# Kernel optimization log

Hardware: AMD Instinct MI355X
Metric: run time of the kernel (lower is better)

The kernel has to match this reference:

```python
import jax, jax.numpy as jnp
import numpy as np

B, C, D, H, K = 512, 112, 128, 8, 8  # batch, channels(=seq), d_model, heads, conv kernel
HD = D // H
SCALE = HD ** -0.5
BN_EPS = 1e-5
LN_EPS = 1e-5


def setup_inputs() -> dict:
    key = jax.random.key(0)
    ks = jax.random.split(key, 12)
    s = 0.05
    return {
        "x": jax.random.normal(ks[0], (B, C, D), jnp.float32),
        "conv_w": jax.random.normal(ks[1], (C, 1, K), jnp.float32) * s,
        "conv_b": jax.random.normal(ks[2], (C,), jnp.float32) * s,
        "bn_g": jnp.ones((C,), jnp.float32),
        "bn_b": jnp.zeros((C,), jnp.float32),
        "bn_m": jnp.zeros((C,), jnp.float32),
        "bn_v": jnp.ones((C,), jnp.float32),
        "wq": jax.random.normal(ks[3], (D, D), jnp.float32) * s,
        "bq": jax.random.normal(ks[4], (D,), jnp.float32) * s,
        "wk": jax.random.normal(ks[5], (D, D), jnp.float32) * s,
        "bk": jax.random.normal(ks[6], (D,), jnp.float32) * s,
        "wv": jax.random.normal(ks[7], (D, D), jnp.float32) * s,
        "bv": jax.random.normal(ks[8], (D,), jnp.float32) * s,
        "wo": jax.random.normal(ks[9], (D, D), jnp.float32) * s,
        "bo": jax.random.normal(ks[10], (D,), jnp.float32) * s,
        "ln_g": jnp.ones((D,), jnp.float32),
        "ln_b": jnp.zeros((D,), jnp.float32),
    }


def _forward(x, conv_w, conv_b, bn_g, bn_b, bn_m, bn_v,
             wq, bq, wk, bk, wv, bv, wo, bo, ln_g, ln_b):
    # resnet_1: depthwise Conv1d(padding='same', k=8) -> GELU -> BatchNorm1d (eval)
    # torch 'same' padding for even k: left = (k-1)//2 = 3, right = 4
    h = jax.lax.conv_general_dilated(
        x, conv_w, window_strides=(1,), padding=[(3, 4)],
        dimension_numbers=("NCH", "OIH", "NCH"), feature_group_count=C)
    h = h + conv_b[None, :, None]
    h = jax.nn.gelu(h, approximate=False)
    h = (h - bn_m[None, :, None]) * (bn_g[None, :, None] * jax.lax.rsqrt(bn_v + BN_EPS)[None, :, None]) + bn_b[None, :, None]
    src = x + h  # [B, C, D]; attention treats C as sequence dim

    # multi-head attention (hand-rolled, res_attention path with prev=None)
    q = (src @ wq.T + bq).reshape(B, C, H, HD).transpose(0, 2, 1, 3)  # [B,H,S,hd]
    k = (src @ wk.T + bk).reshape(B, C, H, HD).transpose(0, 2, 1, 3)
    v = (src @ wv.T + bv).reshape(B, C, H, HD).transpose(0, 2, 1, 3)
    scores = jnp.einsum("bhqd,bhkd->bhqk", q, k) * SCALE  # [B,H,S,S]
    attn = jax.nn.softmax(scores, axis=-1)
    out = jnp.einsum("bhqk,bhkd->bhqd", attn, v)  # [B,H,S,hd]
    out = out.transpose(0, 2, 1, 3).reshape(B, C, D)
    out = out @ wo.T + bo

    # residual + LayerNorm over last dim
    src = src + out
    mu = jnp.mean(src, axis=-1, keepdims=True)
    var = jnp.mean(jnp.square(src - mu), axis=-1, keepdims=True)
    src = (src - mu) * jax.lax.rsqrt(var + LN_EPS) * ln_g + ln_b
    return src


def reference(x, conv_w, conv_b, bn_g, bn_b, bn_m, bn_v,
              wq, bq, wk, bk, wv, bv, wo, bo, ln_g, ln_b):
    return _forward(x, conv_w, conv_b, bn_g, bn_b, bn_m, bn_v,
                    wq, bq, wk, bk, wv, bv, wo, bo, ln_g, ln_b)
```

## Files before the change

### kernel.cpp

```cpp
#include <hip/hip_runtime.h>
#include <hip/hip_bf16.h>

#define BB 512
#define CC 112
#define DD 128
#define HH 8
#define HD 16
#define KK 8
#define SROW 140

typedef unsigned short u16;
typedef short short8 __attribute__((ext_vector_type(8)));
typedef float f32x4 __attribute__((ext_vector_type(4)));
typedef float f32x16 __attribute__((ext_vector_type(16)));

#define MFMA16(a, b, c) __builtin_amdgcn_mfma_f32_16x16x32_bf16(a, b, c, 0, 0, 0)
#define MFMA32(a, b, c) __builtin_amdgcn_mfma_f32_32x32x16_bf16(a, b, c, 0, 0, 0)

#define GLD_LDS16(gsrc, ldst)                                          \
  __builtin_amdgcn_global_load_lds(                                    \
      (const __attribute__((address_space(1))) char*)(gsrc),           \
      (__attribute__((address_space(3))) char*)(ldst), 16, 0, 0)

__device__ inline u16 f2bf(float f) {
  union { float f; unsigned u; } v{f};
  unsigned r = (v.u + 0x7FFFu + ((v.u >> 16) & 1u)) >> 16;
  return (u16)r;
}
__device__ inline float bf2f(u16 u) {
  union { unsigned u; float f; } v;
  v.u = ((unsigned)u) << 16;
  return v.f;
}
__device__ inline unsigned pk2(float a, float b) {
  __hip_bfloat162 h = __float22bfloat162_rn(float2{a, b});
  union { __hip_bfloat162 h; unsigned u; } v{h};
  return v.u;
}

__device__ inline unsigned permx32(unsigned x) {
  unsigned a = x, b = x;
  asm("v_permlane32_swap_b32 %0, %1" : "+v"(a), "+v"(b));
  return (threadIdx.x & 32) ? a : b;
}
__device__ inline float permx32f(float x) {
  union { float f; unsigned u; } v{x};
  v.u = permx32(v.u);
  return v.f;
}

__global__ __launch_bounds__(256) void k_wcvt(
    const float* __restrict__ wq, const float* __restrict__ wk,
    const float* __restrict__ wv, const float* __restrict__ wo,
    u16* __restrict__ w_b) {
  const int i = (blockIdx.x * 256 + threadIdx.x);
  const int sel = i >> 12, off = i & 4095;
  const float* w = (sel == 0) ? wq : (sel == 1) ? wk : (sel == 2) ? wv : wo;
  const float4 v = ((const float4*)w)[off];
  ((uint2*)w_b)[i] = uint2{pk2(v.x, v.y), pk2(v.z, v.w)};
}

__global__ __launch_bounds__(512, 4) void k_cqkv(
    const float* __restrict__ x, const float* __restrict__ cw,
    const float* __restrict__ cb, const float* __restrict__ bg,
    const float* __restrict__ bb_, const float* __restrict__ bm,
    const float* __restrict__ bv, const u16* __restrict__ w_b,
    const float* __restrict__ bq, const float* __restrict__ bk,
    const float* __restrict__ bvv,
    u16* __restrict__ src_b, u16* __restrict__ qb, u16* __restrict__ kb,
    u16* __restrict__ vtb) {
  __shared__ u16 S[CC * SROW];
  const int b = blockIdx.x;
  const int t = threadIdx.x;

  const int tg = t >> 2, sub = t & 3;
  if (tg < CC) {
    const int row = tg, ch = tg;
    const float4 w0 = *(const float4*)(cw + ch * KK);
    const float4 w1 = *(const float4*)(cw + ch * KK + 4);
    const float cbv = cb[ch];
    const float bscale = bg[ch] * rsqrtf(bv[ch] + 1e-5f);
    const float bmv = bm[ch], bbv = bb_[ch];
    const float* __restrict__ xr = x + ((size_t)b * CC + row) * DD;
    float in[40];
#pragma unroll
    for (int f = 0; f < 10; ++f) {
      const int fi = 8 * sub - 1 + f;
      float4 vv = {0.f, 0.f, 0.f, 0.f};
      if (fi >= 0 && fi < 32) vv = ((const float4*)xr)[fi];
      in[f * 4 + 0] = vv.x; in[f * 4 + 1] = vv.y;
      in[f * 4 + 2] = vv.z; in[f * 4 + 3] = vv.w;
    }
    unsigned pkv[16];
#pragma unroll
    for (int i2 = 0; i2 < 16; ++i2) {
      float oo[2];
#pragma unroll
      for (int j = 0; j < 2; ++j) {
        const int i = i2 * 2 + j;
        float a = 0.f;
        a = fmaf(in[i + 1], w0.x, a);
        a = fmaf(in[i + 2], w0.y, a);
        a = fmaf(in[i + 3], w0.z, a);
        a = fmaf(in[i + 4], w0.w, a);
        a = fmaf(in[i + 5], w1.x, a);
        a = fmaf(in[i + 6], w1.y, a);
        a = fmaf(in[i + 7], w1.z, a);
        a = fmaf(in[i + 8], w1.w, a);
        a += cbv;
        const float u = fmaf(0.044715f * a, a, 1.0f);
        const float e = __expf(a * u * -1.5957691216f);
        const float g = a * __frcp_rn(1.f + e);
        oo[j] = in[i + 4] + (g - bmv) * bscale + bbv;
      }
      pkv[i2] = pk2(oo[0], oo[1]);
    }
    u16* srow = S + row * SROW + sub * 32;
#pragma unroll
    for (int k2 = 0; k2 < 8; ++k2)
      *(uint2*)(srow + k2 * 4) = ((uint2*)pkv)[k2];
    uint4* gsr = (uint4*)(src_b + ((size_t)b * CC + row) * DD + sub * 32);
#pragma unroll
    for (int k4 = 0; k4 < 4; ++k4) gsr[k4] = ((uint4*)pkv)[k4];
  }
  __syncthreads();

  const int wave = t >> 6, lane = t & 63;
  const int quad = lane >> 4, n = lane & 15;
  const int h = wave;
  short8 Bf0[4], Bf1[4], Bf2[4];
#pragma unroll
  for (int kf = 0; kf < 4; ++kf) {
    const int wi = (h * 16 + n) * DD + kf * 32 + quad * 8;
    Bf0[kf] = *(const short8*)(w_b + wi);
    Bf1[kf] = *(const short8*)(w_b + 16384 + wi);
    Bf2[kf] = *(const short8*)(w_b + 32768 + wi);
  }
  const float bqv = bq[h * 16 + n];
  const float bkv = bk[h * 16 + n];
  const float bvv2 = bvv[h * 16 + n];
  u16* __restrict__ qhp = qb + (size_t)(b * HH + h) * CC * HD;
  u16* __restrict__ khp = kb + (size_t)(b * HH + h) * CC * HD;
  u16* __restrict__ vhp = vtb + (size_t)(b * HH + h) * HD * CC;
#pragma unroll
  for (int mt = 0; mt < 7; ++mt) {
    short8 A[4];
#pragma unroll
    for (int kf = 0; kf < 4; ++kf)
      A[kf] = *(const short8*)&S[(mt * 16 + n) * SROW + kf * 32 + quad * 8];
    f32x4 aq = {0.f, 0.f, 0.f, 0.f};
    f32x4 ak = {0.f, 0.f, 0.f, 0.f};
    f32x4 av = {0.f, 0.f, 0.f, 0.f};
#pragma unroll
    for (int kf = 0; kf < 4; ++kf) {
      aq = MFMA16(A[kf], Bf0[kf], aq);
      ak = MFMA16(A[kf], Bf1[kf], ak);
      av = MFMA16(A[kf], Bf2[kf], av);
    }
#pragma unroll
    for (int r = 0; r < 4; ++r) {
      const int row = mt * 16 + quad * 4 + r;
      qhp[row * HD + n] = f2bf(aq[r] + bqv);
      khp[row * HD + n] = f2bf(ak[r] + bkv);
      vhp[n * CC + row] = f2bf(av[r] + bvv2);
    }
  }
}

__global__ __launch_bounds__(512, 4) void k_attno(
    const u16* __restrict__ qb_, const u16* __restrict__ kb_,
    const u16* __restrict__ vtb_, const u16* __restrict__ w_bo,
    const float* __restrict__ bo, const u16* __restrict__ src_b,
    const float* __restrict__ lg, const float* __restrict__ lb,
    float* __restrict__ out) {
  __shared__ __attribute__((aligned(16))) u16 KL[HH * CC * HD];
  __shared__ __attribute__((aligned(16))) u16 VL[HH * HD * CC];
  __shared__ u16 AO[64 * SROW];
  const int bid = blockIdx.x;
  const int b = bid & (BB - 1);
  const int hb = bid >> 9;
  const int t = threadIdx.x;
  const int wave = t >> 6, lane = t & 63;

  {
    const char* kg = (const char*)(kb_ + (size_t)b * (HH * CC * HD));
    const char* vg = (const char*)(vtb_ + (size_t)b * (HH * HD * CC));
    char* kl = (char*)KL;
    char* vl = (char*)VL;
#pragma unroll
    for (int c0 = 0; c0 < 4; ++c0) {
      const int c = wave + c0 * 8;
      if (c < 28) {
        GLD_LDS16(kg + c * 1024 + (lane << 4), kl + c * 1024);
        GLD_LDS16(vg + c * 1024 + (lane << 4), vl + c * 1024);
      }
    }
  }
  __syncthreads();

  {
    const int h = wave;
    const int lo = lane & 31, hi = lane >> 5, hi8 = hi * 8;
    const u16* __restrict__ qh = qb_ + (size_t)(b * HH + h) * CC * HD;
    const u16* kh = KL + h * CC * HD;
    const u16* vth = VL + h * HD * CC;
    for (int qi = 0; qi < 2; ++qi) {
      const int qt = 2 * hb + qi;
      const int qt0 = qt * 32;
      short8 Bq = {};
      if (qt0 + lo < CC) Bq = *(const short8*)(qh + (qt0 + lo) * HD + hi8);
      f32x16 sa[4];
#pragma unroll
      for (int mt = 0; mt < 4; ++mt) {
        short8 Ak = {};
        const int key = mt * 32 + lo;
        if (key < CC) Ak = *(const short8*)(kh + key * HD + hi8);
        f32x16 z = {};
        sa[mt] = MFMA32(Ak, Bq, z);
      }
      const float C1 = 0.25f * 1.44269504088896341f;
      float mxp[4] = {-1e30f, -1e30f, -1e30f, -1e30f};
#pragma unroll
      for (int mt = 0; mt < 4; ++mt) {
        const int rmax = (mt == 3) ? 8 : 16;
#pragma unroll
        for (int r = 0; r < 16; ++r)
          if (r < rmax) mxp[r & 3] = fmaxf(mxp[r & 3], sa[mt][r]);
      }
      float mx = fmaxf(fmaxf(mxp[0], mxp[1]), fmaxf(mxp[2], mxp[3]));
      mx = fmaxf(mx, permx32f(mx));
      const float mxc = mx * C1;
      float sp[4] = {0.f, 0.f, 0.f, 0.f};
#pragma unroll
      for (int mt = 0; mt < 4; ++mt) {
        const int rmax = (mt == 3) ? 8 : 16;
#pragma unroll
        for (int r = 0; r < 16; ++r)
          if (r < rmax) {
            const float p = exp2f(fmaf(sa[mt][r], C1, -mxc));
            sa[mt][r] = p;
            sp[r & 3] += p;
          }
      }
      float sum = (sp[0] + sp[1]) + (sp[2] + sp[3]);
      sum += permx32f(sum);
      const float rinv = 1.f / sum;
      unsigned U0[4][4], U1[4][4];
#pragma unroll
      for (int mt = 0; mt < 4; ++mt) {
        const int rqmax = (mt == 3) ? 2 : 4;
#pragma unroll
        for (int rq = 0; rq < 4; ++rq)
          if (rq < rqmax) {
            U0[mt][rq] =
                pk2(sa[mt][4 * rq + 0] * rinv, sa[mt][4 * rq + 1] * rinv);
            U1[mt][rq] =
                pk2(sa[mt][4 * rq + 2] * rinv, sa[mt][4 * rq + 3] * rinv);
          }
      }
      f32x16 oacc = {};
#pragma unroll
      for (int kt = 0; kt < 7; ++kt) {
        const int mt = kt >> 1;
        const int c = 2 * (kt & 1);
        const unsigned own0 = hi ? U0[mt][c + 1] : U0[mt][c];
        const unsigned own1 = hi ? U1[mt][c + 1] : U1[mt][c];
        const unsigned snd0 = hi ? U0[mt][c] : U0[mt][c + 1];
        const unsigned snd1 = hi ? U1[mt][c] : U1[mt][c + 1];
        const unsigned got0 = permx32(snd0);
        const unsigned got1 = permx32(snd1);
        union { unsigned u[4]; short8 s; } ap;
        ap.u[0] = hi ? got0 : own0;
        ap.u[1] = hi ? got1 : own1;
        ap.u[2] = hi ? own0 : got0;
        ap.u[3] = hi ? own1 : got1;
        short8 Bv = {};
        if (lo < HD) Bv = *(const short8*)(vth + lo * CC + kt * 16 + hi8);
        oacc = MFMA32(ap.s, Bv, oacc);
      }
      if (lo < HD) {
#pragma unroll
        for (int r = 0; r < 16; ++r) {
          const int rr = (r & 3) + 8 * (r >> 2) + 4 * hi;
          if (qt0 + rr < CC)
            AO[(qi * 32 + rr) * SROW + h * HD + lo] = f2bf(oacc[r]);
        }
      }
    }
  }
  __syncthreads();

  if (wave < 4) {
    const int mt = 4 * hb + wave;
    if (mt < 7) {
      const int quad = lane >> 4, n = lane & 15;
      short8 A[4];
#pragma unroll
      for (int kf = 0; kf < 4; ++kf)
        A[kf] =
            *(const short8*)&AO[(wave * 16 + n) * SROW + kf * 32 + quad * 8];
      float v[8][4];
#pragma unroll
      for (int nt = 0; nt < 8; ++nt) {
        f32x4 acc = {0.f, 0.f, 0.f, 0.f};
#pragma unroll
        for (int kf = 0; kf < 4; ++kf) {
          const short8 Bf =
              *(const short8*)(w_bo + (nt * 16 + n) * DD + kf * 32 + quad * 8);
          acc = MFMA16(A[kf], Bf, acc);
        }
        const int col = nt * 16 + n;
        const float bcol = bo[col];
#pragma unroll
        for (int r = 0; r < 4; ++r)
          v[nt][r] =
              acc[r] + bcol +
              bf2f(src_b[((size_t)b * CC + mt * 16 + quad * 4 + r) * DD + col]);
      }
      float sum[4] = {0.f, 0.f, 0.f, 0.f}, sq[4] = {0.f, 0.f, 0.f, 0.f};
#pragma unroll
      for (int nt = 0; nt < 8; ++nt)
#pragma unroll
        for (int r = 0; r < 4; ++r) {
          sum[r] += v[nt][r];
          sq[r] = fmaf(v[nt][r], v[nt][r], sq[r]);
        }
#pragma unroll
      for (int d = 1; d < 16; d <<= 1)
#pragma unroll
        for (int r = 0; r < 4; ++r) {
          sum[r] += __shfl_xor(sum[r], d);
          sq[r] += __shfl_xor(sq[r], d);
        }
      float mu[4], rs[4];
#pragma unroll
      for (int r = 0; r < 4; ++r) {
        mu[r] = sum[r] * (1.f / DD);
        const float var = sq[r] * (1.f / DD) - mu[r] * mu[r];
        rs[r] = rsqrtf(var + 1e-5f);
      }
#pragma unroll
      for (int nt = 0; nt < 8; ++nt) {
        const int col = nt * 16 + n;
        const float g = lg[col], be = lb[col];
#pragma unroll
        for (int r = 0; r < 4; ++r)
          out[((size_t)b * CC + mt * 16 + quad * 4 + r) * DD + col] =
              (v[nt][r] - mu[r]) * rs[r] * g + be;
      }
    }
  }
}

extern "C" void kernel_launch(void* const* d_in, const int* in_sizes, int n_in,
                              void* d_out, int out_size, void* d_ws,
                              size_t ws_size, hipStream_t stream) {
  (void)in_sizes; (void)n_in; (void)out_size; (void)ws_size;
  const float* x   = (const float*)d_in[0];
  const float* cw  = (const float*)d_in[1];
  const float* cb  = (const float*)d_in[2];
  const float* bg  = (const float*)d_in[3];
  const float* bb  = (const float*)d_in[4];
  const float* bm  = (const float*)d_in[5];
  const float* bv  = (const float*)d_in[6];
  const float* wq  = (const float*)d_in[7];
  const float* bq  = (const float*)d_in[8];
  const float* wk  = (const float*)d_in[9];
  const float* bk  = (const float*)d_in[10];
  const float* wv  = (const float*)d_in[11];
  const float* bvv = (const float*)d_in[12];
  const float* wo  = (const float*)d_in[13];
  const float* bo  = (const float*)d_in[14];
  const float* lg  = (const float*)d_in[15];
  const float* lb  = (const float*)d_in[16];
  float* out = (float*)d_out;

  const size_t NE = (size_t)BB * CC * DD;
  u16* ub = (u16*)d_ws;
  u16* src_b = ub;
  u16* q_b   = ub + NE;
  u16* k_b   = ub + 2 * NE;
  u16* vt_b  = ub + 3 * NE;
  u16* w_b   = ub + 4 * NE;

  k_wcvt<<<64, 256, 0, stream>>>(wq, wk, wv, wo, w_b);
  k_cqkv<<<BB, 512, 0, stream>>>(x, cw, cb, bg, bb, bm, bv, w_b, bq, bk, bvv,
                                 src_b, q_b, k_b, vt_b);
  k_attno<<<2 * BB, 512, 0, stream>>>(q_b, k_b, vt_b, w_b + 3 * 16384, bo,
                                      src_b, lg, lb, out);
}
```

Baseline: 172.3 us.

## Fuse conv/QKV and attention/out-proj kernels into one per-batch kernel

```diff
diff --git a/kernel.cpp b/kernel.cpp
--- a/kernel.cpp
+++ b/kernel.cpp
@@ -8,6 +8,7 @@
 #define HD 16
 #define KK 8
 #define SROW 140
+#define QS 1792
 
 typedef unsigned short u16;
 typedef short short8 __attribute__((ext_vector_type(8)));
@@ -16,11 +17,6 @@
 
 #define MFMA16(a, b, c) __builtin_amdgcn_mfma_f32_16x16x32_bf16(a, b, c, 0, 0, 0)
 #define MFMA32(a, b, c) __builtin_amdgcn_mfma_f32_32x32x16_bf16(a, b, c, 0, 0, 0)
-
-#define GLD_LDS16(gsrc, ldst)                                          \
-  __builtin_amdgcn_global_load_lds(                                    \
-      (const __attribute__((address_space(1))) char*)(gsrc),           \
-      (__attribute__((address_space(3))) char*)(ldst), 16, 0, 0)
 
 __device__ inline u16 f2bf(float f) {
   union { float f; unsigned u; } v{f};
@@ -60,20 +56,24 @@
   ((uint2*)w_b)[i] = uint2{pk2(v.x, v.y), pk2(v.z, v.w)};
 }
 
-__global__ __launch_bounds__(512, 4) void k_cqkv(
+__global__ __launch_bounds__(1024, 4) void k_fused(
     const float* __restrict__ x, const float* __restrict__ cw,
     const float* __restrict__ cb, const float* __restrict__ bg,
     const float* __restrict__ bb_, const float* __restrict__ bm,
     const float* __restrict__ bv, const u16* __restrict__ w_b,
     const float* __restrict__ bq, const float* __restrict__ bk,
-    const float* __restrict__ bvv,
-    u16* __restrict__ src_b, u16* __restrict__ qb, u16* __restrict__ kb,
-    u16* __restrict__ vtb) {
-  __shared__ u16 S[CC * SROW];
+    const float* __restrict__ bvv, const float* __restrict__ bo,
+    const float* __restrict__ lg, const float* __restrict__ lb,
+    float* __restrict__ out) {
+  __shared__ __attribute__((aligned(16))) u16 S[CC * SROW];
+  __shared__ __attribute__((aligned(16))) u16 QL[HH * CC * HD];
+  __shared__ __attribute__((aligned(16))) u16 KL[HH * CC * HD];
+  __shared__ __attribute__((aligned(16))) u16 VTL[HH * HD * CC];
   const int b = blockIdx.x;
   const int t = threadIdx.x;
-
-  const int tg = t >> 2, sub = t & 3;
+  const int wave = t >> 6, lane = t & 63;
+
+  const int tg = t >> 3, s = t & 7;
   if (tg < CC) {
     const int row = tg, ch = tg;
     const float4 w0 = *(const float4*)(cw + ch * KK);
@@ -82,18 +82,18 @@
     const float bscale = bg[ch] * rsqrtf(bv[ch] + 1e-5f);
     const float bmv = bm[ch], bbv = bb_[ch];
     const float* __restrict__ xr = x + ((size_t)b * CC + row) * DD;
-    float in[40];
-#pragma unroll
-    for (int f = 0; f < 10; ++f) {
-      const int fi = 8 * sub - 1 + f;
+    float in[24];
+#pragma unroll
+    for (int f = 0; f < 6; ++f) {
+      const int fi = 4 * s - 1 + f;
       float4 vv = {0.f, 0.f, 0.f, 0.f};
       if (fi >= 0 && fi < 32) vv = ((const float4*)xr)[fi];
       in[f * 4 + 0] = vv.x; in[f * 4 + 1] = vv.y;
       in[f * 4 + 2] = vv.z; in[f * 4 + 3] = vv.w;
     }
-    unsigned pkv[16];
-#pragma unroll
-    for (int i2 = 0; i2 < 16; ++i2) {
+    unsigned pkv[8];
+#pragma unroll
+    for (int i2 = 0; i2 < 8; ++i2) {
       float oo[2];
 #pragma unroll
       for (int j = 0; j < 2; ++j) {
@@ -115,106 +115,79 @@
       }
       pkv[i2] = pk2(oo[0], oo[1]);
     }
-    u16* srow = S + row * SROW + sub * 32;
-#pragma unroll
-    for (int k2 = 0; k2 < 8; ++k2)
+    u16* srow = S + row * SROW + s * 16;
+#pragma unroll
+    for (int k2 = 0; k2 < 4; ++k2)
       *(uint2*)(srow + k2 * 4) = ((uint2*)pkv)[k2];
-    uint4* gsr = (uint4*)(src_b + ((size_t)b * CC + row) * DD + sub * 32);
-#pragma unroll
-    for (int k4 = 0; k4 < 4; ++k4) gsr[k4] = ((uint4*)pkv)[k4];
   }
   __syncthreads();
 
-  const int wave = t >> 6, lane = t & 63;
-  const int quad = lane >> 4, n = lane & 15;
-  const int h = wave;
-  short8 Bf0[4], Bf1[4], Bf2[4];
-#pragma unroll
-  for (int kf = 0; kf < 4; ++kf) {
-    const int wi = (h * 16 + n) * DD + kf * 32 + quad * 8;
-    Bf0[kf] = *(const short8*)(w_b + wi);
-    Bf1[kf] = *(const short8*)(w_b + 16384 + wi);
-    Bf2[kf] = *(const short8*)(w_b + 32768 + wi);
-  }
-  const float bqv = bq[h * 16 + n];
-  const float bkv = bk[h * 16 + n];
-  const float bvv2 = bvv[h * 16 + n];
-  u16* __restrict__ qhp = qb + (size_t)(b * HH + h) * CC * HD;
-  u16* __restrict__ khp = kb + (size_t)(b * HH + h) * CC * HD;
-  u16* __restrict__ vhp = vtb + (size_t)(b * HH + h) * HD * CC;
-#pragma unroll
-  for (int mt = 0; mt < 7; ++mt) {
-    short8 A[4];
-#pragma unroll
-    for (int kf = 0; kf < 4; ++kf)
-      A[kf] = *(const short8*)&S[(mt * 16 + n) * SROW + kf * 32 + quad * 8];
-    f32x4 aq = {0.f, 0.f, 0.f, 0.f};
-    f32x4 ak = {0.f, 0.f, 0.f, 0.f};
-    f32x4 av = {0.f, 0.f, 0.f, 0.f};
+  {
+    const int h = wave >> 1, mh = wave & 1;
+    const int quad = lane >> 4, n = lane & 15;
+    short8 Bf0[4], Bf1[4], Bf2[4];
 #pragma unroll
     for (int kf = 0; kf < 4; ++kf) {
-      aq = MFMA16(A[kf], Bf0[kf], aq);
-      ak = MFMA16(A[kf], Bf1[kf], ak);
-      av = MFMA16(A[kf], Bf2[kf], av);
-    }
-#pragma unroll
-    for (int r = 0; r < 4; ++r) {
-      const int row = mt * 16 + quad * 4 + r;
-      qhp[row * HD + n] = f2bf(aq[r] + bqv);
-      khp[row * HD + n] = f2bf(ak[r] + bkv);
-      vhp[n * CC + row] = f2bf(av[r] + bvv2);
-    }
-  }
-}
-
-__global__ __launch_bounds__(512, 4) void k_attno(
-    const u16* __restrict__ qb_, const u16* __restrict__ kb_,
-    const u16* __restrict__ vtb_, const u16* __restrict__ w_bo,
-    const float* __restrict__ bo, const u16* __restrict__ src_b,
-    const float* __restrict__ lg, const float* __restrict__ lb,
-    float* __restrict__ out) {
-  __shared__ __attribute__((aligned(16))) u16 KL[HH * CC * HD];
-  __shared__ __attribute__((aligned(16))) u16 VL[HH * HD * CC];
-  __shared__ u16 AO[64 * SROW];
-  const int bid = blockIdx.x;
-  const int b = bid & (BB - 1);
-  const int hb = bid >> 9;
-  const int t = threadIdx.x;
-  const int wave = t >> 6, lane = t & 63;
-
-  {
-    const char* kg = (const char*)(kb_ + (size_t)b * (HH * CC * HD));
-    const char* vg = (const char*)(vtb_ + (size_t)b * (HH * HD * CC));
-    char* kl = (char*)KL;
-    char* vl = (char*)VL;
-#pragma unroll
-    for (int c0 = 0; c0 < 4; ++c0) {
-      const int c = wave + c0 * 8;
-      if (c < 28) {
-        GLD_LDS16(kg + c * 1024 + (lane << 4), kl + c * 1024);
-        GLD_LDS16(vg + c * 1024 + (lane << 4), vl + c * 1024);
+      const int wi = (h * 16 + n) * DD + kf * 32 + quad * 8;
+      Bf0[kf] = *(const short8*)(w_b + wi);
+      Bf1[kf] = *(const short8*)(w_b + 16384 + wi);
+      Bf2[kf] = *(const short8*)(w_b + 32768 + wi);
+    }
+    const float bqv = bq[h * 16 + n];
+    const float bkv = bk[h * 16 + n];
+    const float bvv2 = bvv[h * 16 + n];
+    u16* qlh = QL + h * QS;
+    u16* klh = KL + h * QS;
+    u16* vlh = VTL + h * QS;
+#pragma unroll
+    for (int m = 0; m < 4; ++m) {
+      const int mt = mh * 4 + m;
+      if (mt < 7) {
+        short8 A[4];
+#pragma unroll
+        for (int kf = 0; kf < 4; ++kf)
+          A[kf] = *(const short8*)&S[(mt * 16 + n) * SROW + kf * 32 + quad * 8];
+        f32x4 aq = {0.f, 0.f, 0.f, 0.f};
+        f32x4 ak = {0.f, 0.f, 0.f, 0.f};
+        f32x4 av = {0.f, 0.f, 0.f, 0.f};
+#pragma unroll
+        for (int kf = 0; kf < 4; ++kf) {
+          aq = MFMA16(A[kf], Bf0[kf], aq);
+          ak = MFMA16(A[kf], Bf1[kf], ak);
+          av = MFMA16(A[kf], Bf2[kf], av);
+        }
+        const int row0 = mt * 16 + quad * 4;
+#pragma unroll
+        for (int r = 0; r < 4; ++r) {
+          qlh[(row0 + r) * HD + n] = f2bf(aq[r] + bqv);
+          klh[(row0 + r) * HD + n] = f2bf(ak[r] + bkv);
+        }
+        *(uint2*)&vlh[n * CC + row0] =
+            uint2{pk2(av[0] + bvv2, av[1] + bvv2),
+                  pk2(av[2] + bvv2, av[3] + bvv2)};
       }
     }
   }
   __syncthreads();
 
   {
-    const int h = wave;
+    const int h = wave >> 1, qh = wave & 1;
     const int lo = lane & 31, hi = lane >> 5, hi8 = hi * 8;
-    const u16* __restrict__ qh = qb_ + (size_t)(b * HH + h) * CC * HD;
-    const u16* kh = KL + h * CC * HD;
-    const u16* vth = VL + h * HD * CC;
+    const u16* qlh = QL + h * QS;
+    const u16* klh = KL + h * QS;
+    const u16* vlh = VTL + h * QS;
+    u16* aoh = QL + h * QS;
     for (int qi = 0; qi < 2; ++qi) {
-      const int qt = 2 * hb + qi;
+      const int qt = qh * 2 + qi;
       const int qt0 = qt * 32;
       short8 Bq = {};
-      if (qt0 + lo < CC) Bq = *(const short8*)(qh + (qt0 + lo) * HD + hi8);
+      if (qt0 + lo < CC) Bq = *(const short8*)(qlh + (qt0 + lo) * HD + hi8);
       f32x16 sa[4];
 #pragma unroll
       for (int mt = 0; mt < 4; ++mt) {
         short8 Ak = {};
         const int key = mt * 32 + lo;
-        if (key < CC) Ak = *(const short8*)(kh + key * HD + hi8);
+        if (key < CC) Ak = *(const short8*)(klh + key * HD + hi8);
         f32x16 z = {};
         sa[mt] = MFMA32(Ak, Bq, z);
       }
@@ -275,79 +248,77 @@
         ap.u[2] = hi ? own0 : got0;
         ap.u[3] = hi ? own1 : got1;
         short8 Bv = {};
-        if (lo < HD) Bv = *(const short8*)(vth + lo * CC + kt * 16 + hi8);
+        if (lo < HD) Bv = *(const short8*)(vlh + lo * CC + kt * 16 + hi8);
         oacc = MFMA32(ap.s, Bv, oacc);
       }
       if (lo < HD) {
 #pragma unroll
         for (int r = 0; r < 16; ++r) {
           const int rr = (r & 3) + 8 * (r >> 2) + 4 * hi;
-          if (qt0 + rr < CC)
-            AO[(qi * 32 + rr) * SROW + h * HD + lo] = f2bf(oacc[r]);
+          if (qt0 + rr < CC) aoh[(qt0 + rr) * HD + lo] = f2bf(oacc[r]);
         }
       }
     }
   }
   __syncthreads();
 
-  if (wave < 4) {
-    const int mt = 4 * hb + wave;
-    if (mt < 7) {
-      const int quad = lane >> 4, n = lane & 15;
-      short8 A[4];
-#pragma unroll
-      for (int kf = 0; kf < 4; ++kf)
-        A[kf] =
-            *(const short8*)&AO[(wave * 16 + n) * SROW + kf * 32 + quad * 8];
-      float v[8][4];
-#pragma unroll
-      for (int nt = 0; nt < 8; ++nt) {
-        f32x4 acc = {0.f, 0.f, 0.f, 0.f};
-#pragma unroll
-        for (int kf = 0; kf < 4; ++kf) {
-          const short8 Bf =
-              *(const short8*)(w_bo + (nt * 16 + n) * DD + kf * 32 + quad * 8);
-          acc = MFMA16(A[kf], Bf, acc);
-        }
-        const int col = nt * 16 + n;
-        const float bcol = bo[col];
-#pragma unroll
-        for (int r = 0; r < 4; ++r)
-          v[nt][r] =
-              acc[r] + bcol +
-              bf2f(src_b[((size_t)b * CC + mt * 16 + quad * 4 + r) * DD + col]);
-      }
-      float sum[4] = {0.f, 0.f, 0.f, 0.f}, sq[4] = {0.f, 0.f, 0.f, 0.f};
-#pragma unroll
-      for (int nt = 0; nt < 8; ++nt)
-#pragma unroll
-        for (int r = 0; r < 4; ++r) {
-          sum[r] += v[nt][r];
-          sq[r] = fmaf(v[nt][r], v[nt][r], sq[r]);
-        }
-#pragma unroll
-      for (int d = 1; d < 16; d <<= 1)
-#pragma unroll
-        for (int r = 0; r < 4; ++r) {
-          sum[r] += __shfl_xor(sum[r], d);
-          sq[r] += __shfl_xor(sq[r], d);
-        }
-      float mu[4], rs[4];
+  if (wave < 7) {
+    const int quad = lane >> 4, n = lane & 15;
+    const int mt = wave;
+    const u16* __restrict__ w_bo = w_b + 3 * 16384;
+    short8 A[4];
+#pragma unroll
+    for (int kf = 0; kf < 4; ++kf) {
+      const int head = 2 * kf + (quad >> 1);
+      A[kf] = *(const short8*)&QL[head * QS + (mt * 16 + n) * HD + (quad & 1) * 8];
+    }
+    float v[8][4];
+#pragma unroll
+    for (int nt = 0; nt < 8; ++nt) {
+      f32x4 acc = {0.f, 0.f, 0.f, 0.f};
+#pragma unroll
+      for (int kf = 0; kf < 4; ++kf) {
+        const short8 Bf =
+            *(const short8*)(w_bo + (nt * 16 + n) * DD + kf * 32 + quad * 8);
+        acc = MFMA16(A[kf], Bf, acc);
+      }
+      const int col = nt * 16 + n;
+      const float bcol = bo[col];
+#pragma unroll
+      for (int r = 0; r < 4; ++r)
+        v[nt][r] = acc[r] + bcol +
+                   bf2f(S[(mt * 16 + quad * 4 + r) * SROW + col]);
+    }
+    float sum[4] = {0.f, 0.f, 0.f, 0.f}, sq[4] = {0.f, 0.f, 0.f, 0.f};
+#pragma unroll
+    for (int nt = 0; nt < 8; ++nt)
 #pragma unroll
       for (int r = 0; r < 4; ++r) {
-        mu[r] = sum[r] * (1.f / DD);
-        const float var = sq[r] * (1.f / DD) - mu[r] * mu[r];
-        rs[r] = rsqrtf(var + 1e-5f);
-      }
-#pragma unroll
-      for (int nt = 0; nt < 8; ++nt) {
-        const int col = nt * 16 + n;
-        const float g = lg[col], be = lb[col];
-#pragma unroll
-        for (int r = 0; r < 4; ++r)
-          out[((size_t)b * CC + mt * 16 + quad * 4 + r) * DD + col] =
-              (v[nt][r] - mu[r]) * rs[r] * g + be;
-      }
+        sum[r] += v[nt][r];
+        sq[r] = fmaf(v[nt][r], v[nt][r], sq[r]);
+      }
+#pragma unroll
+    for (int d = 1; d < 16; d <<= 1)
+#pragma unroll
+      for (int r = 0; r < 4; ++r) {
+        sum[r] += __shfl_xor(sum[r], d);
+        sq[r] += __shfl_xor(sq[r], d);
+      }
+    float mu[4], rs[4];
+#pragma unroll
+    for (int r = 0; r < 4; ++r) {
+      mu[r] = sum[r] * (1.f / DD);
+      const float var = sq[r] * (1.f / DD) - mu[r] * mu[r];
+      rs[r] = rsqrtf(var + 1e-5f);
+    }
+#pragma unroll
+    for (int nt = 0; nt < 8; ++nt) {
+      const int col = nt * 16 + n;
+      const float g = lg[col], be = lb[col];
+#pragma unroll
+      for (int r = 0; r < 4; ++r)
+        out[((size_t)b * CC + mt * 16 + quad * 4 + r) * DD + col] =
+            (v[nt][r] - mu[r]) * rs[r] * g + be;
     }
   }
 }
@@ -375,17 +346,9 @@
   const float* lb  = (const float*)d_in[16];
   float* out = (float*)d_out;
 
-  const size_t NE = (size_t)BB * CC * DD;
-  u16* ub = (u16*)d_ws;
-  u16* src_b = ub;
-  u16* q_b   = ub + NE;
-  u16* k_b   = ub + 2 * NE;
-  u16* vt_b  = ub + 3 * NE;
-  u16* w_b   = ub + 4 * NE;
+  u16* w_b = (u16*)d_ws;
 
   k_wcvt<<<64, 256, 0, stream>>>(wq, wk, wv, wo, w_b);
-  k_cqkv<<<BB, 512, 0, stream>>>(x, cw, cb, bg, bb, bm, bv, w_b, bq, bk, bvv,
-                                 src_b, q_b, k_b, vt_b);
-  k_attno<<<2 * BB, 512, 0, stream>>>(q_b, k_b, vt_b, w_b + 3 * 16384, bo,
-                                      src_b, lg, lb, out);
-}
+  k_fused<<<BB, 1024, 0, stream>>>(x, cw, cb, bg, bb, bm, bv, w_b, bq, bk,
+                                   bvv, bo, lg, lb, out);
+}
```

Result: no change. 173.3 us (+0.6%).
